# Performance work log

Hardware: AMD Instinct MI355X
Metric: run time of the kernel (lower is better)

The kernel has to match this reference:

```python
import jax, jax.numpy as jnp
import numpy as np

T, N, E, H, G, P = 8, 512, 64, 128, 4, 128
NS = 2.0  # neighbourhood_size


def _init(k, shape):
    fan_in = shape[-1]
    return jax.random.normal(k, shape, jnp.float32) / jnp.sqrt(jnp.float32(fan_in))


def setup_inputs() -> dict:
    key = jax.random.key(0)
    ks = jax.random.split(key, 12)
    return {
        "observed": jax.random.normal(ks[0], (T, N, 2), jnp.float32),
        "W_pos": _init(ks[1], (E, 2)), "b_pos": jnp.zeros((E,), jnp.float32),
        "W_pool": _init(ks[2], (P, G * G * H)), "b_pool": jnp.zeros((P,), jnp.float32),
        "W_ih_enc": _init(ks[3], (4 * H, E + P)), "b_ih_enc": jnp.zeros((4 * H,), jnp.float32),
        "W_hh_enc": _init(ks[4], (4 * H, H)), "b_hh_enc": jnp.zeros((4 * H,), jnp.float32),
        "W_ih_dec": _init(ks[5], (4 * H, E + P)), "b_ih_dec": jnp.zeros((4 * H,), jnp.float32),
        "W_hh_dec": _init(ks[6], (4 * H, H)), "b_hh_dec": jnp.zeros((4 * H,), jnp.float32),
        "W_out": _init(ks[7], (2, H)), "b_out": jnp.zeros((2,), jnp.float32),
        "n_predict": 12,
    }


def _impute(observed):
    # backfill leading gaps, forward-fill later gaps, zeros if never valid
    Tn, n, _ = observed.shape
    finite = jnp.isfinite(observed).all(-1)                       # [T,N]
    idx = jnp.where(finite, jnp.arange(Tn)[:, None], -1)
    last = jax.lax.associative_scan(jnp.maximum, idx, axis=0)     # last valid t' <= t
    first = jnp.argmax(finite, axis=0)                            # first valid t
    take = jnp.where(last >= 0, last, first[None, :])             # [T,N]
    obs = jnp.take_along_axis(observed, jnp.broadcast_to(take[:, :, None], (Tn, n, 2)), axis=0)
    return jnp.where(finite.any(0)[None, :, None], obs, 0.0)


def _social_pool(pos, hidden, W_pool, b_pool):
    # grid-cell binning + per-cell max pooling of neighbour hidden states
    n, h = hidden.shape
    half, cell = NS / 2.0, NS / G
    rel = pos[None, :, :] - pos[:, None, :]                       # [N,N,2] pos[j]-pos[i]
    fin_pos = jnp.isfinite(pos).all(-1)
    fin_hid = jnp.isfinite(hidden).all(-1)
    inr = (jnp.abs(rel) <= half).all(-1)
    eye = jnp.eye(n, dtype=bool)
    mask = inr & fin_pos[:, None] & fin_pos[None, :] & fin_hid[None, :] & (~eye)
    g = jnp.clip(jnp.floor((rel + half) / cell).astype(jnp.int32), 0, G - 1)  # [N,N,2]
    cid = g[..., 0] * G + g[..., 1]                               # gx*G+gy layout
    seg = jnp.where(mask, jnp.arange(n, dtype=jnp.int32)[:, None] * (G * G) + cid, n * G * G)
    seg = seg.reshape(-1)                                         # [N*N]
    data = jnp.broadcast_to(hidden[None], (n, n, h)).reshape(n * n, h)
    pooled = jax.ops.segment_max(data, seg, num_segments=n * G * G + 1)[: n * G * G]
    counts = jax.ops.segment_sum(jnp.ones((n * n,), jnp.float32), seg, num_segments=n * G * G + 1)[: n * G * G]
    pooled = jnp.where(counts[:, None] > 0, pooled, 0.0)          # empty cells -> zero_hidden
    grid = pooled.reshape(n, G * G * h)
    return jax.nn.relu(grid @ W_pool.T + b_pool)


def reference(observed, W_pos, b_pos, W_pool, b_pool,
              W_ih_enc, b_ih_enc, W_hh_enc, b_hh_enc,
              W_ih_dec, b_ih_dec, W_hh_dec, b_hh_dec,
              W_out, b_out, n_predict):
    obs = _impute(observed)
    n = obs.shape[1]

    def step(W_ih, b_ih, W_hh, b_hh, hs, cs, pos, prev):
        vel = pos - prev
        emb = jax.nn.relu(vel @ W_pos.T + b_pos)
        soc = _social_pool(pos, hs, W_pool, b_pool)
        x = jnp.concatenate([emb, soc], axis=1)
        gates = x @ W_ih.T + b_ih + hs @ W_hh.T + b_hh
        i, f, gg, o = jnp.split(gates, 4, axis=1)
        cs2 = jax.nn.sigmoid(f) * cs + jax.nn.sigmoid(i) * jnp.tanh(gg)
        hs2 = jax.nn.sigmoid(o) * jnp.tanh(cs2)
        nxt = pos + hs2 @ W_out.T + b_out
        return hs2, cs2, nxt

    def enc_step(carry, inp):
        hs, cs = carry
        pos, prev = inp
        hs, cs, _ = step(W_ih_enc, b_ih_enc, W_hh_enc, b_hh_enc, hs, cs, pos, prev)
        return (hs, cs), None

    hs = jnp.zeros((n, H), jnp.float32)
    cs = jnp.zeros((n, H), jnp.float32)
    (hs, cs), _ = jax.lax.scan(enc_step, (hs, cs), (obs[1:], obs[:-1]))

    def dec_step(carry, _):
        hs, cs, prev, curr = carry
        hs, cs, nxt = step(W_ih_dec, b_ih_dec, W_hh_dec, b_hh_dec, hs, cs, curr, prev)
        return (hs, cs, jax.lax.stop_gradient(curr), jax.lax.stop_gradient(nxt)), nxt

    _, preds = jax.lax.scan(dec_step, (hs, cs, obs[-1], obs[-1]), None, length=int(n_predict))
    return preds  # [n_predict, N, 2]
```

## Files before the change

kernel.cpp:

```cpp
#include <hip/hip_runtime.h>
#include <math.h>

#define NBLK 256
#define NTHR 512

#define OFF_OBS     8256
#define OFF_PART    16448
#define OFF_WTPOOL  540736
#define OFF_WTG_E   802880
#define OFF_WTG_D   966720
#define OFF_HSBUF   1130560

#define LDS_BYTES 31232

typedef float vf4 __attribute__((ext_vector_type(4)));
typedef float vf2 __attribute__((ext_vector_type(2)));

__device__ __forceinline__ int asr20(int row) { return row * 20 + ((row >> 5) << 2); }

__device__ __forceinline__ void st_bypass_f4(float* p, vf4 v) {
    asm volatile("global_store_dwordx4 %0, %1, off sc0 sc1" :: "v"(p), "v"(v) : "memory");
}
__device__ __forceinline__ void st_bypass_f2(float* p, vf2 v) {
    asm volatile("global_store_dwordx2 %0, %1, off sc0 sc1" :: "v"(p), "v"(v) : "memory");
}
__device__ __forceinline__ void ld_bypass_f4x8(const float* b, int stride, vf4* v) {
    asm volatile(
        "global_load_dwordx4 %0, %8, off sc0 sc1\n\t"
        "global_load_dwordx4 %1, %9, off sc0 sc1\n\t"
        "global_load_dwordx4 %2, %10, off sc0 sc1\n\t"
        "global_load_dwordx4 %3, %11, off sc0 sc1\n\t"
        "global_load_dwordx4 %4, %12, off sc0 sc1\n\t"
        "global_load_dwordx4 %5, %13, off sc0 sc1\n\t"
        "global_load_dwordx4 %6, %14, off sc0 sc1\n\t"
        "global_load_dwordx4 %7, %15, off sc0 sc1\n\t"
        "s_waitcnt vmcnt(0)"
        : "=&v"(v[0]), "=&v"(v[1]), "=&v"(v[2]), "=&v"(v[3]),
          "=&v"(v[4]), "=&v"(v[5]), "=&v"(v[6]), "=&v"(v[7])
        : "v"(b), "v"(b + stride), "v"(b + 2 * stride), "v"(b + 3 * stride),
          "v"(b + 4 * stride), "v"(b + 5 * stride), "v"(b + 6 * stride), "v"(b + 7 * stride)
        : "memory");
}

__device__ __forceinline__ void grid_barrier_fenced(unsigned* flags, unsigned* gen, unsigned seq) {
    __syncthreads();
    if (threadIdx.x == 0)
        __builtin_amdgcn_fence(__ATOMIC_RELEASE, "agent");
    if (blockIdx.x == 0) {
        if (threadIdx.x < 64) {
            #pragma unroll
            for (int q = 0; q < 4; q++) {
                int bb = threadIdx.x * 4 + q;
                if (bb != 0) {
                    while (__hip_atomic_load(&flags[bb * 16], __ATOMIC_RELAXED,
                                             __HIP_MEMORY_SCOPE_AGENT) != seq)
                        __builtin_amdgcn_s_sleep(1);
                }
            }
        }
        __syncthreads();
        if (threadIdx.x == 0) {
            __hip_atomic_store(gen, seq, __ATOMIC_RELAXED, __HIP_MEMORY_SCOPE_AGENT);
            __builtin_amdgcn_fence(__ATOMIC_ACQUIRE, "agent");
        }
    } else {
        if (threadIdx.x == 0) {
            __hip_atomic_store(&flags[blockIdx.x * 16], seq, __ATOMIC_RELAXED,
                               __HIP_MEMORY_SCOPE_AGENT);
            while (__hip_atomic_load(gen, __ATOMIC_RELAXED,
                                     __HIP_MEMORY_SCOPE_AGENT) != seq)
                __builtin_amdgcn_s_sleep(2);
            __builtin_amdgcn_fence(__ATOMIC_ACQUIRE, "agent");
        }
    }
    __syncthreads();
}

__device__ __forceinline__ void grid_barrier_nf(unsigned* flags, unsigned* gen, unsigned seq) {
    __syncthreads();
    if (blockIdx.x == 0) {
        if (threadIdx.x < 64) {
            #pragma unroll
            for (int q = 0; q < 4; q++) {
                int bb = threadIdx.x * 4 + q;
                if (bb != 0) {
                    while (__hip_atomic_load(&flags[bb * 16], __ATOMIC_RELAXED,
                                             __HIP_MEMORY_SCOPE_AGENT) != seq)
                        __builtin_amdgcn_s_sleep(1);
                }
            }
        }
        __syncthreads();
        if (threadIdx.x == 0)
            __hip_atomic_store(gen, seq, __ATOMIC_RELAXED, __HIP_MEMORY_SCOPE_AGENT);
    } else {
        if (threadIdx.x == 0) {
            __hip_atomic_store(&flags[blockIdx.x * 16], seq, __ATOMIC_RELAXED,
                               __HIP_MEMORY_SCOPE_AGENT);
            while (__hip_atomic_load(gen, __ATOMIC_RELAXED,
                                     __HIP_MEMORY_SCOPE_AGENT) != seq)
                __builtin_amdgcn_s_sleep(2);
        }
    }
    __syncthreads();
}

__device__ __forceinline__ float sigm(float x) { return 1.f / (1.f + expf(-x)); }

__global__ void __launch_bounds__(NTHR, 1) social_lstm(
    const float* __restrict__ observed,
    const float* __restrict__ W_pos, const float* __restrict__ b_pos,
    const float* __restrict__ W_pool, const float* __restrict__ b_pool,
    const float* __restrict__ Wih_e, const float* __restrict__ bih_e,
    const float* __restrict__ Whh_e, const float* __restrict__ bhh_e,
    const float* __restrict__ Wih_d, const float* __restrict__ bih_d,
    const float* __restrict__ Whh_d, const float* __restrict__ bhh_d,
    const float* __restrict__ W_out, const float* __restrict__ b_out,
    float* __restrict__ out, float* __restrict__ ws, int npred)
{
    extern __shared__ char smem_raw[];
    const int t = threadIdx.x, b = blockIdx.x;
    const int gid = b * NTHR + t;

    unsigned* flags  = (unsigned*)ws;
    unsigned* gen    = flags + 4096;
    unsigned* rtf    = flags + 4112;
    float* obs     = ws + OFF_OBS;
    float* part    = ws + OFF_PART;
    float* Wt_pool = ws + OFF_WTPOOL;
    float* Wt_ge   = ws + OFF_WTG_E;
    float* Wt_gd   = ws + OFF_WTG_D;
    float* hsbuf   = ws + OFF_HSBUF;
    unsigned seq = 1;

    if (gid < 65536) hsbuf[gid] = 0.f;
    if (gid < 512) {
        float vx[8], vy[8];
        int fin = 0;
        for (int tt = 0; tt < 8; tt++) {
            float x = observed[tt * 1024 + gid * 2];
            float y = observed[tt * 1024 + gid * 2 + 1];
            vx[tt] = x; vy[tt] = y;
            if (isfinite(x) && isfinite(y)) fin |= (1 << tt);
        }
        int firstv = -1;
        for (int tt = 7; tt >= 0; tt--) if (fin & (1 << tt)) firstv = tt;
        int last = -1;
        for (int tt = 0; tt < 8; tt++) {
            if (fin & (1 << tt)) last = tt;
            int take = (last >= 0) ? last : firstv;
            float ox = 0.f, oy = 0.f;
            if (take >= 0) { ox = vx[take]; oy = vy[take]; }
            obs[tt * 1024 + gid * 2]     = ox;
            obs[tt * 1024 + gid * 2 + 1] = oy;
        }
    }
    if (gid < 65536) {
        int p = gid >> 9, k4 = gid & 511;
        float4 v = *(const float4*)(W_pool + p * 2048 + k4 * 4);
        float* dst = Wt_pool + (k4 * 4) * 128 + p;
        dst[0] = v.x; dst[128] = v.y; dst[256] = v.z; dst[384] = v.w;
    }
    for (int idx = gid; idx < 163840; idx += NBLK * NTHR) {
        int k = idx >> 9, o = idx & 511;
        float ve, vd;
        if (k < 192) { ve = Wih_e[o * 192 + k];       vd = Wih_d[o * 192 + k]; }
        else         { ve = Whh_e[o * 128 + k - 192]; vd = Whh_d[o * 128 + k - 192]; }
        Wt_ge[idx] = ve; Wt_gd[idx] = vd;
    }
    grid_barrier_fenced(flags, gen, seq++);

    const int rt = b >> 3, kc = b & 7, hc = kc;
    const int R0 = rt * 16;
    float cs_reg = 0.f;
    const int nstep = 7 + npred;

    for (int s = 0; s < nstep; s++) {
        const float* posp  = (s < 7) ? (obs + (s + 1) * 1024)
                                     : ((s == 7) ? (obs + 7 * 1024) : (out + (s - 8) * 1024));
        const float* prevp = (s < 7) ? (obs + s * 1024)
                                     : ((s <= 8) ? (obs + 7 * 1024) : (out + (s - 9) * 1024));
        const float* Wt_g = (s < 7) ? Wt_ge : Wt_gd;
        const float* bihp = (s < 7) ? bih_e : bih_d;
        const float* bhhp = (s < 7) ? bhh_e : bhh_d;
        const float* hs_r = hsbuf + s * 65536;
        float*       hs_w = hsbuf + (s + 1) * 65536;

        {
            float* pos2 = (float*)smem_raw;
            int* cnt    = (int*)(smem_raw + 4096);
            unsigned short* lst = (unsigned short*)(smem_raw + 4224);
            float* AsT  = (float*)(smem_raw + 10368);

            if (t < 256) ((float4*)pos2)[t] = ((const float4*)posp)[t];
            if (t < 32) cnt[t] = 0;
            __syncthreads();

            if (kc == 1 && s >= 7 && t < 16) {
                int i = R0 + t;
                vf2 v;
                v.x = pos2[2 * i] + b_out[0];
                v.y = pos2[2 * i + 1] + b_out[1];
                st_bypass_f2(out + (s - 7) * 1024 + 2 * i, v);
            }
            {
                int a = t >> 5, i = R0 + a;
                float pix = pos2[2 * i], piy = pos2[2 * i + 1];
                int c0 = kc * 2;
                for (int jj = 0; jj < 16; jj++) {
                    int j = (t & 31) + jj * 32;
                    float dx = pos2[2 * j]     - pix;
                    float dy = pos2[2 * j + 1] - piy;
                    if (j != i && fabsf(dx) <= 1.0f && fabsf(dy) <= 1.0f) {
                        int gx = (int)floorf((dx + 1.0f) * 2.0f); gx = gx < 0 ? 0 : (gx > 3 ? 3 : gx);
                        int gy = (int)floorf((dy + 1.0f) * 2.0f); gy = gy < 0 ? 0 : (gy > 3 ? 3 : gy);
                        int cc = gx * 4 + gy - c0;
                        if (cc == 0 || cc == 1) {
                            int slot = atomicAdd(&cnt[a * 2 + cc], 1);
                            if (slot < 96) lst[(a * 2 + cc) * 96 + slot] = (unsigned short)j;
                        }
                    }
                }
            }
            __syncthreads();
            {
                int a = t >> 5, cc = (t >> 4) & 1, hq = t & 15;
                int len = cnt[a * 2 + cc]; if (len > 96) len = 96;
                float m[8];
                #pragma unroll
                for (int u = 0; u < 8; u++) m[u] = -3.0e38f;
                const unsigned short* ll = lst + (a * 2 + cc) * 96;
                for (int e = 0; e < len; e += 8) {
                    float4 va[8], vb[8];
                    #pragma unroll
                    for (int k2 = 0; k2 < 8; k2++) {
                        int ee = e + k2; if (ee >= len) ee = len - 1;
                        const float4* hp = (const float4*)(hs_r + (int)ll[ee] * 128 + hq * 8);
                        va[k2] = hp[0]; vb[k2] = hp[1];
                    }
                    #pragma unroll
                    for (int k2 = 0; k2 < 8; k2++) {
                        m[0] = fmaxf(m[0], va[k2].x); m[1] = fmaxf(m[1], va[k2].y);
                        m[2] = fmaxf(m[2], va[k2].z); m[3] = fmaxf(m[3], va[k2].w);
                        m[4] = fmaxf(m[4], vb[k2].x); m[5] = fmaxf(m[5], vb[k2].y);
                        m[6] = fmaxf(m[6], vb[k2].z); m[7] = fmaxf(m[7], vb[k2].w);
                    }
                }
                #pragma unroll
                for (int u = 0; u < 8; u++)
                    AsT[asr20(cc * 128 + hq * 8 + u) + a] = (len > 0) ? m[u] : 0.f;
            }
            __syncthreads();
            {
                int og = (t & 7) | (((t >> 6) & 1) << 3);
                int ks = (t >> 3) & 7;
                int rowg = t >> 7;
                float acc[4][8];
                #pragma unroll
                for (int r = 0; r < 4; r++)
                    #pragma unroll
                    for (int o = 0; o < 8; o++) acc[r][o] = 0.f;
                const float4* W4 = (const float4*)Wt_pool;
                int kb = kc * 256 + ks * 32;
                #pragma unroll 4
                for (int kk = 0; kk < 32; kk++) {
                    int kl = ks * 32 + kk;
                    float4 a4 = *(const float4*)&AsT[asr20(kl) + rowg * 4];
                    float4 w0 = W4[(kb + kk) * 32 + og * 2];
                    float4 w1 = W4[(kb + kk) * 32 + og * 2 + 1];
                    float ar[4] = {a4.x, a4.y, a4.z, a4.w};
                    float wo[8] = {w0.x, w0.y, w0.z, w0.w, w1.x, w1.y, w1.z, w1.w};
                    #pragma unroll
                    for (int r = 0; r < 4; r++)
                        #pragma unroll
                        for (int o = 0; o < 8; o++)
                            acc[r][o] = fmaf(ar[r], wo[o], acc[r][o]);
                }
                #pragma unroll
                for (int r = 0; r < 4; r++)
                    #pragma unroll
                    for (int o = 0; o < 8; o++) {
                        acc[r][o] += __shfl_xor(acc[r][o], 8);
                        acc[r][o] += __shfl_xor(acc[r][o], 16);
                        acc[r][o] += __shfl_xor(acc[r][o], 32);
                    }
                if ((t & 56) == 0) {
                    #pragma unroll
                    for (int r = 0; r < 4; r++) {
                        int row = R0 + rowg * 4 + r;
                        float* pp = part + kc * 65536 + row * 128 + og * 8;
                        vf4 lo, hi;
                        lo.x = acc[r][0]; lo.y = acc[r][1]; lo.z = acc[r][2]; lo.w = acc[r][3];
                        hi.x = acc[r][4]; hi.y = acc[r][5]; hi.z = acc[r][6]; hi.w = acc[r][7];
                        st_bypass_f4(pp,     lo);
                        st_bypass_f4(pp + 4, hi);
                    }
                }
            }
        }

        __syncthreads();
        if (t == 0)
            __hip_atomic_store(&rtf[(rt * 8 + kc) * 16], (unsigned)(s + 1),
                               __ATOMIC_RELAXED, __HIP_MEMORY_SCOPE_AGENT);
        {
            float* AsT  = (float*)smem_raw;
            {
                int r = t >> 5, e2 = (t & 31) * 2;
                int i2 = 2 * (R0 + r);
                float vx = posp[i2]     - prevp[i2];
                float vy = posp[i2 + 1] - prevp[i2 + 1];
                float e0 = fmaxf(W_pos[e2 * 2]     * vx + W_pos[e2 * 2 + 1] * vy + b_pos[e2],     0.f);
                float e1 = fmaxf(W_pos[e2 * 2 + 2] * vx + W_pos[e2 * 2 + 3] * vy + b_pos[e2 + 1], 0.f);
                AsT[asr20(e2 + 0) + r] = e0;
                AsT[asr20(e2 + 1) + r] = e1;
            }
            {
                int r = t >> 5, h4 = (t & 31) * 4;
                float4 v = *(const float4*)(hs_r + (R0 + r) * 128 + h4);
                AsT[asr20(192 + h4 + 0) + r] = v.x;
                AsT[asr20(192 + h4 + 1) + r] = v.y;
                AsT[asr20(192 + h4 + 2) + r] = v.z;
                AsT[asr20(192 + h4 + 3) + r] = v.w;
            }
            if (t < 8) {
                while (__hip_atomic_load(&rtf[(rt * 8 + t) * 16], __ATOMIC_RELAXED,
                                         __HIP_MEMORY_SCOPE_AGENT) != (unsigned)(s + 1))
                    __builtin_amdgcn_s_sleep(1);
            }
            __syncthreads();
            {
                int r = t >> 5, p4 = (t & 31) * 4;
                vf4 pv[8];
                ld_bypass_f4x8(part + (R0 + r) * 128 + p4, 65536, pv);
                float sv[4] = {0.f, 0.f, 0.f, 0.f};
                #pragma unroll
                for (int kc2 = 0; kc2 < 8; kc2++) {
                    sv[0] += pv[kc2].x; sv[1] += pv[kc2].y;
                    sv[2] += pv[kc2].z; sv[3] += pv[kc2].w;
                }
                #pragma unroll
                for (int u = 0; u < 4; u++)
                    AsT[asr20(64 + p4 + u) + r] = fmaxf(sv[u] + b_pool[p4 + u], 0.f);
            }
            __syncthreads();
            float* red  = (float*)(smem_raw + 25792);
            float* hrow = (float*)(smem_raw + 29888);
            {
                int og = (t & 7) | (((t >> 6) & 1) << 3);
                int ks = (t >> 3) & 7;
                int rowg = t >> 7;
                int col4 = (og >> 2) * 32 + hc * 4 + (og & 3);
                float acc[4][4];
                #pragma unroll
                for (int r = 0; r < 4; r++)
                    #pragma unroll
                    for (int o = 0; o < 4; o++) acc[r][o] = 0.f;
                const float4* Wg4 = (const float4*)Wt_g;
                #pragma unroll 4
                for (int kk = 0; kk < 40; kk++) {
                    int k = ks * 40 + kk;
                    float4 a4 = *(const float4*)&AsT[asr20(k) + rowg * 4];
                    float4 w  = Wg4[k * 128 + col4];
                    float ar[4] = {a4.x, a4.y, a4.z, a4.w};
                    float wo[4] = {w.x, w.y, w.z, w.w};
                    #pragma unroll
                    for (int r = 0; r < 4; r++)
                        #pragma unroll
                        for (int o = 0; o < 4; o++)
                            acc[r][o] = fmaf(ar[r], wo[o], acc[r][o]);
                }
                #pragma unroll
                for (int r = 0; r < 4; r++)
                    #pragma unroll
                    for (int o = 0; o < 4; o++) {
                        acc[r][o] += __shfl_xor(acc[r][o], 8);
                        acc[r][o] += __shfl_xor(acc[r][o], 16);
                        acc[r][o] += __shfl_xor(acc[r][o], 32);
                    }
                if ((t & 56) == 0) {
                    #pragma unroll
                    for (int r = 0; r < 4; r++)
                        *(float4*)&red[(rowg * 4 + r) * 64 + og * 4] =
                            make_float4(acc[r][0], acc[r][1], acc[r][2], acc[r][3]);
                }
            }
            __syncthreads();
            if (t < 256) {
                int rl = t >> 4, hh = t & 15;
                float g4[4];
                #pragma unroll
                for (int q = 0; q < 4; q++) {
                    int colq = q * 128 + hc * 16 + hh;
                    g4[q] = red[rl * 64 + q * 16 + hh] + bihp[colq] + bhhp[colq];
                }
                float si = sigm(g4[0]);
                float sf = sigm(g4[1]);
                float so = sigm(g4[3]);
                float c2 = sf * cs_reg + si * tanhf(g4[2]);
                float h2 = so * tanhf(c2);
                cs_reg = c2;
                hrow[rl * 16 + hh] = h2;
                if (s >= 7) {
                    int i = R0 + rl, h = hc * 16 + hh;
                    float v0 = W_out[h] * h2;
                    float v1 = W_out[128 + h] * h2;
                    v0 += __shfl_down(v0, 8); v0 += __shfl_down(v0, 4);
                    v0 += __shfl_down(v0, 2); v0 += __shfl_down(v0, 1);
                    v1 += __shfl_down(v1, 8); v1 += __shfl_down(v1, 4);
                    v1 += __shfl_down(v1, 2); v1 += __shfl_down(v1, 1);
                    if (hh == 0) {
                        atomicAdd(&out[(s - 7) * 1024 + 2 * i],     v0);
                        atomicAdd(&out[(s - 7) * 1024 + 2 * i + 1], v1);
                    }
                }
            }
            __syncthreads();
            if (t < 64) {
                int rl = t >> 2, q = t & 3;
                vf4 v;
                v.x = hrow[rl * 16 + q * 4 + 0];
                v.y = hrow[rl * 16 + q * 4 + 1];
                v.z = hrow[rl * 16 + q * 4 + 2];
                v.w = hrow[rl * 16 + q * 4 + 3];
                st_bypass_f4(hs_w + (R0 + rl) * 128 + hc * 16 + q * 4, v);
            }
        }
        grid_barrier_nf(flags, gen, seq++);
    }
}

extern "C" void kernel_launch(void* const* d_in, const int* in_sizes, int n_in,
                              void* d_out, int out_size, void* d_ws, size_t ws_size,
                              hipStream_t stream) {
    const float* observed = (const float*)d_in[0];
    const float* W_pos    = (const float*)d_in[1];
    const float* b_pos    = (const float*)d_in[2];
    const float* W_pool   = (const float*)d_in[3];
    const float* b_pool   = (const float*)d_in[4];
    const float* Wih_e    = (const float*)d_in[5];
    const float* bih_e    = (const float*)d_in[6];
    const float* Whh_e    = (const float*)d_in[7];
    const float* bhh_e    = (const float*)d_in[8];
    const float* Wih_d    = (const float*)d_in[9];
    const float* bih_d    = (const float*)d_in[10];
    const float* Whh_d    = (const float*)d_in[11];
    const float* bhh_d    = (const float*)d_in[12];
    const float* W_out    = (const float*)d_in[13];
    const float* b_out    = (const float*)d_in[14];
    float* outp = (float*)d_out;
    float* wsp  = (float*)d_ws;
    int npred = out_size / 1024;

    hipMemsetAsync(d_ws, 0, 33024, stream);

    social_lstm<<<NBLK, NTHR, LDS_BYTES, stream>>>(
        observed, W_pos, b_pos, W_pool, b_pool,
        Wih_e, bih_e, Whh_e, bhh_e,
        Wih_d, bih_d, Whh_d, bhh_d,
        W_out, b_out, outp, wsp, npred);
}
```

Baseline: 606.5 us.

## Double threads per block and re-split pooling, projection and gate work per thread

Raises the block size from 512 to 1024 threads and re-partitions each phase so every thread handles less: neighbour scan over 8 instead of 16 strided candidates, max-pooling over 4 hidden values instead of 8, pool projection with 4 output columns, and gate GEMM with 2 columns via float2 weight loads. The intent is to shorten the per-step critical path of the latency-bound, grid-synchronised recurrent loop by spreading work over more wavefronts. In exchange it brings more per-thread reduction/shuffle overhead and narrower memory accesses, and some phases leave half the threads idle.

After: 735.0 us. 1.21x slower.

```diff
diff --git a/kernel.cpp b/kernel.cpp
--- a/kernel.cpp
+++ b/kernel.cpp
@@ -2,7 +2,7 @@
 #include <math.h>
 
 #define NBLK 256
-#define NTHR 512
+#define NTHR 1024
 
 #define OFF_OBS     8256
 #define OFF_PART    16448
@@ -107,7 +107,7 @@
 
 __device__ __forceinline__ float sigm(float x) { return 1.f / (1.f + expf(-x)); }
 
-__global__ void __launch_bounds__(NTHR, 1) social_lstm(
+__global__ void __launch_bounds__(NTHR, 4) social_lstm(
     const float* __restrict__ observed,
     const float* __restrict__ W_pos, const float* __restrict__ b_pos,
     const float* __restrict__ W_pool, const float* __restrict__ b_pool,
@@ -161,12 +161,12 @@
         float* dst = Wt_pool + (k4 * 4) * 128 + p;
         dst[0] = v.x; dst[128] = v.y; dst[256] = v.z; dst[384] = v.w;
     }
-    for (int idx = gid; idx < 163840; idx += NBLK * NTHR) {
-        int k = idx >> 9, o = idx & 511;
+    if (gid < 163840) {
+        int k = gid >> 9, o = gid & 511;
         float ve, vd;
         if (k < 192) { ve = Wih_e[o * 192 + k];       vd = Wih_d[o * 192 + k]; }
         else         { ve = Whh_e[o * 128 + k - 192]; vd = Whh_d[o * 128 + k - 192]; }
-        Wt_ge[idx] = ve; Wt_gd[idx] = vd;
+        Wt_ge[gid] = ve; Wt_gd[gid] = vd;
     }
     grid_barrier_fenced(flags, gen, seq++);
 
@@ -204,11 +204,11 @@
                 st_bypass_f2(out + (s - 7) * 1024 + 2 * i, v);
             }
             {
-                int a = t >> 5, i = R0 + a;
+                int a = t >> 6, i = R0 + a;
                 float pix = pos2[2 * i], piy = pos2[2 * i + 1];
                 int c0 = kc * 2;
-                for (int jj = 0; jj < 16; jj++) {
-                    int j = (t & 31) + jj * 32;
+                for (int jj = 0; jj < 8; jj++) {
+                    int j = (t & 63) + jj * 64;
                     float dx = pos2[2 * j]     - pix;
                     float dy = pos2[2 * j + 1] - piy;
                     if (j != i && fabsf(dx) <= 1.0f && fabsf(dy) <= 1.0f) {
@@ -224,62 +224,58 @@
             }
             __syncthreads();
             {
-                int a = t >> 5, cc = (t >> 4) & 1, hq = t & 15;
+                int a = t >> 6, cc = (t >> 5) & 1, q4 = t & 31;
                 int len = cnt[a * 2 + cc]; if (len > 96) len = 96;
-                float m[8];
-                #pragma unroll
-                for (int u = 0; u < 8; u++) m[u] = -3.0e38f;
+                float m[4];
+                #pragma unroll
+                for (int u = 0; u < 4; u++) m[u] = -3.0e38f;
                 const unsigned short* ll = lst + (a * 2 + cc) * 96;
                 for (int e = 0; e < len; e += 8) {
-                    float4 va[8], vb[8];
+                    float4 va[8];
                     #pragma unroll
                     for (int k2 = 0; k2 < 8; k2++) {
                         int ee = e + k2; if (ee >= len) ee = len - 1;
-                        const float4* hp = (const float4*)(hs_r + (int)ll[ee] * 128 + hq * 8);
-                        va[k2] = hp[0]; vb[k2] = hp[1];
+                        va[k2] = *(const float4*)(hs_r + (int)ll[ee] * 128 + q4 * 4);
                     }
                     #pragma unroll
                     for (int k2 = 0; k2 < 8; k2++) {
                         m[0] = fmaxf(m[0], va[k2].x); m[1] = fmaxf(m[1], va[k2].y);
                         m[2] = fmaxf(m[2], va[k2].z); m[3] = fmaxf(m[3], va[k2].w);
-                        m[4] = fmaxf(m[4], vb[k2].x); m[5] = fmaxf(m[5], vb[k2].y);
-                        m[6] = fmaxf(m[6], vb[k2].z); m[7] = fmaxf(m[7], vb[k2].w);
-                    }
-                }
-                #pragma unroll
-                for (int u = 0; u < 8; u++)
-                    AsT[asr20(cc * 128 + hq * 8 + u) + a] = (len > 0) ? m[u] : 0.f;
+                    }
+                }
+                #pragma unroll
+                for (int u = 0; u < 4; u++)
+                    AsT[asr20(cc * 128 + q4 * 4 + u) + a] = (len > 0) ? m[u] : 0.f;
             }
             __syncthreads();
             {
-                int og = (t & 7) | (((t >> 6) & 1) << 3);
+                int og = (t & 7) | (((t >> 6) & 3) << 3);
                 int ks = (t >> 3) & 7;
-                int rowg = t >> 7;
-                float acc[4][8];
+                int rowg = t >> 8;
+                float acc[4][4];
                 #pragma unroll
                 for (int r = 0; r < 4; r++)
                     #pragma unroll
-                    for (int o = 0; o < 8; o++) acc[r][o] = 0.f;
+                    for (int o = 0; o < 4; o++) acc[r][o] = 0.f;
                 const float4* W4 = (const float4*)Wt_pool;
                 int kb = kc * 256 + ks * 32;
                 #pragma unroll 4
                 for (int kk = 0; kk < 32; kk++) {
                     int kl = ks * 32 + kk;
                     float4 a4 = *(const float4*)&AsT[asr20(kl) + rowg * 4];
-                    float4 w0 = W4[(kb + kk) * 32 + og * 2];
-                    float4 w1 = W4[(kb + kk) * 32 + og * 2 + 1];
+                    float4 w  = W4[(kb + kk) * 32 + og];
                     float ar[4] = {a4.x, a4.y, a4.z, a4.w};
-                    float wo[8] = {w0.x, w0.y, w0.z, w0.w, w1.x, w1.y, w1.z, w1.w};
+                    float wo[4] = {w.x, w.y, w.z, w.w};
                     #pragma unroll
                     for (int r = 0; r < 4; r++)
                         #pragma unroll
-                        for (int o = 0; o < 8; o++)
+                        for (int o = 0; o < 4; o++)
                             acc[r][o] = fmaf(ar[r], wo[o], acc[r][o]);
                 }
                 #pragma unroll
                 for (int r = 0; r < 4; r++)
                     #pragma unroll
-                    for (int o = 0; o < 8; o++) {
+                    for (int o = 0; o < 4; o++) {
                         acc[r][o] += __shfl_xor(acc[r][o], 8);
                         acc[r][o] += __shfl_xor(acc[r][o], 16);
                         acc[r][o] += __shfl_xor(acc[r][o], 32);
@@ -288,12 +284,10 @@
                     #pragma unroll
                     for (int r = 0; r < 4; r++) {
                         int row = R0 + rowg * 4 + r;
-                        float* pp = part + kc * 65536 + row * 128 + og * 8;
-                        vf4 lo, hi;
-                        lo.x = acc[r][0]; lo.y = acc[r][1]; lo.z = acc[r][2]; lo.w = acc[r][3];
-                        hi.x = acc[r][4]; hi.y = acc[r][5]; hi.z = acc[r][6]; hi.w = acc[r][7];
-                        st_bypass_f4(pp,     lo);
-                        st_bypass_f4(pp + 4, hi);
+                        float* pp = part + kc * 65536 + row * 128 + og * 4;
+                        vf4 v;
+                        v.x = acc[r][0]; v.y = acc[r][1]; v.z = acc[r][2]; v.w = acc[r][3];
+                        st_bypass_f4(pp, v);
                     }
                 }
             }
@@ -305,7 +299,7 @@
                                __ATOMIC_RELAXED, __HIP_MEMORY_SCOPE_AGENT);
         {
             float* AsT  = (float*)smem_raw;
-            {
+            if (t < 512) {
                 int r = t >> 5, e2 = (t & 31) * 2;
                 int i2 = 2 * (R0 + r);
                 float vx = posp[i2]     - prevp[i2];
@@ -314,9 +308,9 @@
                 float e1 = fmaxf(W_pos[e2 * 2 + 2] * vx + W_pos[e2 * 2 + 3] * vy + b_pos[e2 + 1], 0.f);
                 AsT[asr20(e2 + 0) + r] = e0;
                 AsT[asr20(e2 + 1) + r] = e1;
-            }
-            {
-                int r = t >> 5, h4 = (t & 31) * 4;
+            } else {
+                int t2 = t - 512;
+                int r = t2 >> 5, h4 = (t2 & 31) * 4;
                 float4 v = *(const float4*)(hs_r + (R0 + r) * 128 + h4);
                 AsT[asr20(192 + h4 + 0) + r] = v.x;
                 AsT[asr20(192 + h4 + 1) + r] = v.y;
@@ -329,7 +323,7 @@
                     __builtin_amdgcn_s_sleep(1);
             }
             __syncthreads();
-            {
+            if (t < 512) {
                 int r = t >> 5, p4 = (t & 31) * 4;
                 vf4 pv[8];
                 ld_bypass_f4x8(part + (R0 + r) * 128 + p4, 65536, pv);
@@ -347,33 +341,31 @@
             float* red  = (float*)(smem_raw + 25792);
             float* hrow = (float*)(smem_raw + 29888);
             {
-                int og = (t & 7) | (((t >> 6) & 1) << 3);
+                int og = (t & 7) | (((t >> 6) & 3) << 3);
                 int ks = (t >> 3) & 7;
-                int rowg = t >> 7;
-                int col4 = (og >> 2) * 32 + hc * 4 + (og & 3);
-                float acc[4][4];
-                #pragma unroll
-                for (int r = 0; r < 4; r++)
-                    #pragma unroll
-                    for (int o = 0; o < 4; o++) acc[r][o] = 0.f;
-                const float4* Wg4 = (const float4*)Wt_g;
+                int rowg = t >> 8;
+                int gate = og >> 3, loc = og & 7;
+                int col2 = gate * 64 + hc * 8 + loc;
+                float acc[4][2];
+                #pragma unroll
+                for (int r = 0; r < 4; r++) { acc[r][0] = 0.f; acc[r][1] = 0.f; }
+                const float2* Wg2 = (const float2*)Wt_g;
                 #pragma unroll 4
                 for (int kk = 0; kk < 40; kk++) {
                     int k = ks * 40 + kk;
                     float4 a4 = *(const float4*)&AsT[asr20(k) + rowg * 4];
-                    float4 w  = Wg4[k * 128 + col4];
+                    float2 w  = Wg2[k * 256 + col2];
                     float ar[4] = {a4.x, a4.y, a4.z, a4.w};
-                    float wo[4] = {w.x, w.y, w.z, w.w};
-                    #pragma unroll
-                    for (int r = 0; r < 4; r++)
-                        #pragma unroll
-                        for (int o = 0; o < 4; o++)
-                            acc[r][o] = fmaf(ar[r], wo[o], acc[r][o]);
+                    #pragma unroll
+                    for (int r = 0; r < 4; r++) {
+                        acc[r][0] = fmaf(ar[r], w.x, acc[r][0]);
+                        acc[r][1] = fmaf(ar[r], w.y, acc[r][1]);
+                    }
                 }
                 #pragma unroll
                 for (int r = 0; r < 4; r++)
                     #pragma unroll
-                    for (int o = 0; o < 4; o++) {
+                    for (int o = 0; o < 2; o++) {
                         acc[r][o] += __shfl_xor(acc[r][o], 8);
                         acc[r][o] += __shfl_xor(acc[r][o], 16);
                         acc[r][o] += __shfl_xor(acc[r][o], 32);
@@ -381,8 +373,8 @@
                 if ((t & 56) == 0) {
                     #pragma unroll
                     for (int r = 0; r < 4; r++)
-                        *(float4*)&red[(rowg * 4 + r) * 64 + og * 4] =
-                            make_float4(acc[r][0], acc[r][1], acc[r][2], acc[r][3]);
+                        *(float2*)&red[(rowg * 4 + r) * 64 + gate * 16 + loc * 2] =
+                            make_float2(acc[r][0], acc[r][1]);
                 }
             }
             __syncthreads();
```
